# Optimization experiments

Measured on AMD Instinct MI355X. Metric: run time of the kernel, lower is better.

The kernel has to match this reference:

```python
import jax, jax.numpy as jnp
import numpy as np

N_CLASS, EMB, HID = 32000, 256, 512
B, T = 256, 256


def setup_inputs() -> dict:
    key = jax.random.key(0)
    ks = iter(jax.random.split(key, 64))

    def g(shape, scale=0.02):
        return jax.random.normal(next(ks), shape, jnp.float32) * scale

    inp = {
        "X": jax.random.randint(next(ks), (B, T), 0, N_CLASS),
        "H": g((B, HID)),
        "C": g((B, HID)),
        "E": g((N_CLASS, EMB)),
    }
    # two stacked LSTM cells, gates i/f/o/c; weights stored [in, out] so y = x @ W
    for name in ["i", "f", "o", "c"]:
        inp["W_x" + name] = g((EMB, HID))
        inp["W_h" + name] = g((HID, HID))
        inp["b_" + name] = jnp.ones((HID,), jnp.float32)
        inp["W_x" + name + "1"] = g((EMB, HID))
        inp["W_h" + name + "1"] = g((HID, HID))
        inp["b_" + name + "1"] = jnp.ones((HID,), jnp.float32)
    inp["W_xh"] = g((HID, HID))
    inp["W_hh"] = g((HID, HID))
    inp["b_h"] = jnp.ones((HID,), jnp.float32)
    inp["W_hq"] = g((HID, N_CLASS))
    inp["b_q"] = jnp.ones((N_CLASS,), jnp.float32)
    return inp


def reference(X, H, C, E,
              W_xi, W_hi, b_i, W_xf, W_hf, b_f, W_xo, W_ho, b_o, W_xc, W_hc, b_c,
              W_xi1, W_hi1, b_i1, W_xf1, W_hf1, b_f1, W_xo1, W_ho1, b_o1, W_xc1, W_hc1, b_c1,
              W_xh, W_hh, b_h, W_hq, b_q):
    xs = jnp.swapaxes(E[X], 0, 1)  # [T, B, EMB] time-major, like X.transpose(0,1)

    def step(carry, x_t):
        H, C, H1, C1 = carry
        # first LSTM cell
        I = jax.nn.sigmoid(x_t @ W_xi + H @ W_hi + b_i)
        F = jax.nn.sigmoid(x_t @ W_xf + H @ W_hf + b_f)
        O = jax.nn.sigmoid(x_t @ W_xo + H @ W_ho + b_o)
        Ct = jnp.tanh(x_t @ W_xc + H @ W_hc + b_c)
        C = F * C + I * Ct
        H = O * jnp.tanh(C)
        # inter-layer gated mix (note: H1 is overwritten before the 2nd cell, as in the original)
        H1 = jax.nn.sigmoid(H @ W_xh + H1 @ W_hh + b_h)
        # second LSTM cell
        I1 = jax.nn.sigmoid(x_t @ W_xi1 + H1 @ W_hi1 + b_i1)
        F1 = jax.nn.sigmoid(x_t @ W_xf1 + H1 @ W_hf1 + b_f1)
        O1 = jax.nn.sigmoid(x_t @ W_xo1 + H1 @ W_ho1 + b_o1)
        Ct1 = jnp.tanh(x_t @ W_xc1 + H1 @ W_hc1 + b_c1)
        C1 = F1 * C1 + I1 * Ct1
        H1 = O1 * jnp.tanh(C1)
        return (H, C, H1, C1), None

    # H1 and C1 are initialized from H and C (H1 = H; C1 = C in the original)
    (H, C, H1, C1), _ = jax.lax.scan(step, (H, C, H, C), xs)
    return H1 @ W_hq + b_q  # [B, N_CLASS]
```

## Files before the change

### kernel.cpp

```cpp
#include <hip/hip_runtime.h>
#include <cstdint>
#include <cstddef>

typedef unsigned short u16;
typedef unsigned long long u64;
typedef __attribute__((ext_vector_type(8))) short s16x8;
typedef __attribute__((ext_vector_type(4))) float f32x4;
typedef __attribute__((ext_vector_type(4))) unsigned short u16x4;

#define AGENT __HIP_MEMORY_SCOPE_AGENT

namespace {
constexpr int NWG  = 256;
constexpr int NTHR = 256;
constexpr int Bb   = 256;
constexpr int Tt   = 256;
constexpr int EMB_ = 256;
constexpr int HID_ = 512;
constexpr int NCLS = 32000;

constexpr int OFF_W1  = 0;
constexpr int OFF_W3  = 49152;
constexpr int OFF_W2  = 98304;
constexpr int OFF_DS  = 131072;
constexpr int OFF_DS1 = 139520;
constexpr int OFF_DSM = 147968;
constexpr int OFF_C   = 150144;
constexpr int OFF_C1  = 152192;
constexpr int OFF_B1  = 154240;
constexpr int OFF_B3  = 154368;
constexpr int OFF_B2  = 154496;
constexpr int SMEM_BYTES = 154560;

constexpr size_t WS_FL   = 0;
constexpr size_t WS_DONE = 32768;
constexpr size_t WS_HB0  = 33792;
constexpr size_t WS_HB1  = WS_HB0 + (size_t)Bb * HID_ * 2;
constexpr size_t WS_H1   = WS_HB1 + (size_t)Bb * HID_ * 2;
constexpr size_t WS_HM   = WS_H1 + (size_t)Bb * HID_ * 2;
constexpr size_t WS_XE   = WS_HM + (size_t)Bb * HID_ * 2;
}

struct Params {
  const int* X; const float* Hin; const float* Cin; const float* E;
  const float* Wx[4];  const float* Wh[4];  const float* bg[4];
  const float* Wx1[4]; const float* Wh1[4]; const float* bg1[4];
  const float* Wxh; const float* Whh; const float* bh;
  const float* Whq; const float* bq;
  float* out; char* ws;
};

__device__ __forceinline__ u16 f2bf(float f) {
  union { float f; unsigned u; } v; v.f = f;
  unsigned r = v.u + 0x7FFFu + ((v.u >> 16) & 1u);
  return (u16)(r >> 16);
}
__device__ __forceinline__ float sigm(float x) { return 1.f / (1.f + __expf(-x)); }
__device__ __forceinline__ float tanh_(float x) {
  x = fminf(fmaxf(x, -10.f), 10.f);
  float e = __expf(-2.f * x);
  return (1.f - e) / (1.f + e);
}
__device__ __forceinline__ f32x4 mfma16(s16x8 a, s16x8 b, f32x4 c) {
  return __builtin_amdgcn_mfma_f32_16x16x32_bf16(a, b, c, 0, 0, 0);
}

__device__ __forceinline__ void st8_llc(u16* p2, u64 v) {
  __hip_atomic_store((u64*)p2, v, __ATOMIC_RELAXED, AGENT);
}

#define LD16A(d, b, off)                                                      \
  asm volatile("global_load_dwordx4 %0, %1, off offset:" #off " sc0 sc1"      \
               : "=&v"(d) : "v"(b) : "memory")

__device__ __forceinline__ void ld_h16(s16x8* d, const u16* b) {
  LD16A(d[0],  b, 0);   LD16A(d[1],  b, 64);  LD16A(d[2],  b, 128);
  LD16A(d[3],  b, 192); LD16A(d[4],  b, 256); LD16A(d[5],  b, 320);
  LD16A(d[6],  b, 384); LD16A(d[7],  b, 448); LD16A(d[8],  b, 512);
  LD16A(d[9],  b, 576); LD16A(d[10], b, 640); LD16A(d[11], b, 704);
  LD16A(d[12], b, 768); LD16A(d[13], b, 832); LD16A(d[14], b, 896);
  LD16A(d[15], b, 960);
}
__device__ __forceinline__ void waitld() {
  asm volatile("s_waitcnt vmcnt(0)" ::: "memory");
  __builtin_amdgcn_sched_barrier(0);
}

__device__ __forceinline__ void arrive_cnt(int* fl, int c) {
  __syncthreads();
  if (threadIdx.x == 0)
    (void)__hip_atomic_fetch_add(&fl[(c & 7) * 32 + 16], 1, __ATOMIC_RELAXED, AGENT);
}
__device__ __forceinline__ void wait_cnt(int* fl, int ph) {
  const int tgt = ph * 8;
  if (threadIdx.x < 8) {
    for (;;) {
      int v = __hip_atomic_load(&fl[threadIdx.x * 32 + 16], __ATOMIC_RELAXED, AGENT);
      if (!__any(v < tgt)) break;
      __builtin_amdgcn_s_sleep(1);
    }
  }
  __syncthreads();
  __builtin_amdgcn_fence(__ATOMIC_ACQUIRE, "workgroup");
}

__device__ __forceinline__ void groupbar_heavy(int* fl, int slot, int ph) {
  __syncthreads();
  if (threadIdx.x == 0)
    __hip_atomic_store(&fl[slot * 32], ph, __ATOMIC_RELEASE, AGENT);
  if (threadIdx.x < 64) {
    for (;;) {
      int v = __hip_atomic_load(&fl[threadIdx.x * 32], __ATOMIC_RELAXED, AGENT);
      if (!__any(v < ph)) break;
      __builtin_amdgcn_s_sleep(1);
    }
  }
  __syncthreads();
  __builtin_amdgcn_fence(__ATOMIC_ACQUIRE, "agent");
}

__device__ __forceinline__ void donebar(int* dn, int bi) {
  __syncthreads();
  if (threadIdx.x == 0)
    __hip_atomic_store(&dn[bi], 1, __ATOMIC_RELEASE, AGENT);
  for (;;) {
    int v = __hip_atomic_load(&dn[threadIdx.x], __ATOMIC_RELAXED, AGENT);
    if (!__any(v < 1)) break;
    __builtin_amdgcn_s_sleep(1);
  }
  __syncthreads();
  __builtin_amdgcn_fence(__ATOMIC_ACQUIRE, "agent");
}

__device__ __forceinline__ void cell_phase(char* smem, int offW, int offB, int offC,
                                           const u16* Xt, const u16* Hrec, u16* Hdst,
                                           int g, int c, int w, int lane, int tid) {
  const int r = lane & 15, q = lane >> 4;
  const int row0 = w * 16;
  const u16* xrow = Xt + (size_t)(g * 64 + row0 + r) * EMB_;
  const u16* hrow = Hrec + (size_t)(g * 64 + row0 + r) * HID_;
  const u16* wb = (const u16*)(smem + offW) + lane * 8;
  f32x4 acc0 = {0.f, 0.f, 0.f, 0.f}, acc1 = {0.f, 0.f, 0.f, 0.f};
#pragma unroll
  for (int kb = 0; kb < 8; kb++) {
    s16x8 a  = *(const s16x8*)(xrow + kb * 32 + q * 8);
    s16x8 b0 = *(const s16x8*)(wb + (size_t)(kb * 2 + 0) * 512);
    s16x8 b1 = *(const s16x8*)(wb + (size_t)(kb * 2 + 1) * 512);
    acc0 = mfma16(a, b0, acc0);
    acc1 = mfma16(a, b1, acc1);
  }
  s16x8 ha[16];
  ld_h16(ha, hrow + q * 8);
  waitld();
#pragma unroll
  for (int kb = 0; kb < 16; kb++) {
    s16x8 b0 = *(const s16x8*)(wb + (size_t)((kb + 8) * 2 + 0) * 512);
    s16x8 b1 = *(const s16x8*)(wb + (size_t)((kb + 8) * 2 + 1) * 512);
    acc0 = mfma16(ha[kb], b0, acc0);
    acc1 = mfma16(ha[kb], b1, acc1);
  }
  float* Ds = (float*)(smem + OFF_DS);
#pragma unroll
  for (int i = 0; i < 4; i++) {
    Ds[(row0 + q * 4 + i) * 33 + r]      = acc0[i];
    Ds[(row0 + q * 4 + i) * 33 + 16 + r] = acc1[i];
  }
  __syncthreads();
  const float* bs = (const float*)(smem + offB);
  float* Cs = (float*)(smem + offC);
  if (tid < 128) {
    int row = tid >> 1, j0 = (tid & 1) * 4;
    union { u16 h[4]; u64 qv; } pk;
#pragma unroll
    for (int i = 0; i < 4; i++) {
      int j = j0 + i;
      float vi = Ds[row * 33 + 0 + j]  + bs[0 + j];
      float vf = Ds[row * 33 + 8 + j]  + bs[8 + j];
      float vo = Ds[row * 33 + 16 + j] + bs[16 + j];
      float vc = Ds[row * 33 + 24 + j] + bs[24 + j];
      float I = sigm(vi), F = sigm(vf), O = sigm(vo), Ct = tanh_(vc);
      float Cn = F * Cs[row * 8 + j] + I * Ct;
      Cs[row * 8 + j] = Cn;
      pk.h[i] = f2bf(O * tanh_(Cn));
    }
    st8_llc(Hdst + (size_t)(g * 64 + row) * HID_ + c * 8 + j0, pk.qv);
  }
}

__device__ __forceinline__ void cell1_w23(char* smem, const u16* Xt, const u16* Hrec,
                                          u16* Hdst, int g, int c, int lane, int tid) {
  const int wv = (tid >> 6) - 2;
  const int r = lane & 15, q = lane >> 4;
  const u16* wb1 = (const u16*)(smem + OFF_W1) + lane * 8;
  float* D1 = (float*)(smem + OFF_DS1);
#pragma unroll
  for (int blk = 0; blk < 2; blk++) {
    const int rb = wv * 32 + blk * 16;
    const u16* xrow = Xt + (size_t)(g * 64 + rb + r) * EMB_;
    const u16* hrow = Hrec + (size_t)(g * 64 + rb + r) * HID_;
    s16x8 xa[8];
#pragma unroll
    for (int kb = 0; kb < 8; kb++) xa[kb] = *(const s16x8*)(xrow + kb * 32 + q * 8);
    s16x8 hh[16];
    ld_h16(hh, hrow + q * 8);
    f32x4 a0 = {0.f, 0.f, 0.f, 0.f}, a1 = {0.f, 0.f, 0.f, 0.f};
#pragma unroll
    for (int kb = 0; kb < 8; kb++) {
      a0 = mfma16(xa[kb], *(const s16x8*)(wb1 + (size_t)(kb * 2 + 0) * 512), a0);
      a1 = mfma16(xa[kb], *(const s16x8*)(wb1 + (size_t)(kb * 2 + 1) * 512), a1);
    }
    waitld();
#pragma unroll
    for (int kb = 0; kb < 16; kb++) {
      a0 = mfma16(hh[kb], *(const s16x8*)(wb1 + (size_t)((kb + 8) * 2 + 0) * 512), a0);
      a1 = mfma16(hh[kb], *(const s16x8*)(wb1 + (size_t)((kb + 8) * 2 + 1) * 512), a1);
    }
#pragma unroll
    for (int i = 0; i < 4; i++) {
      D1[(rb + q * 4 + i) * 33 + r]      = a0[i];
      D1[(rb + q * 4 + i) * 33 + 16 + r] = a1[i];
    }
  }
  const float* bs = (const float*)(smem + OFF_B1);
  float* Cs = (float*)(smem + OFF_C);
  int t2 = tid - 128;
  int row = t2 >> 1, j0 = (t2 & 1) * 4;
  union { u16 h[4]; u64 qv; } pk;
#pragma unroll
  for (int i = 0; i < 4; i++) {
    int j = j0 + i;
    float vi = D1[row * 33 + 0 + j]  + bs[0 + j];
    float vf = D1[row * 33 + 8 + j]  + bs[8 + j];
    float vo = D1[row * 33 + 16 + j] + bs[16 + j];
    float vc = D1[row * 33 + 24 + j] + bs[24 + j];
    float I = sigm(vi), F = sigm(vf), O = sigm(vo), Ct = tanh_(vc);
    float Cn = F * Cs[row * 8 + j] + I * Ct;
    Cs[row * 8 + j] = Cn;
    pk.h[i] = f2bf(O * tanh_(Cn));
  }
  st8_llc(Hdst + (size_t)(g * 64 + row) * HID_ + c * 8 + j0, pk.qv);
}

__device__ __forceinline__ f32x4 mix_part1(char* smem, const u16* Hnew, int g, int c,
                                           int w, int lane) {
  const int r = lane & 15, q = lane >> 4;
  int rbase = g * 64 + (c & 1) * 32 + w * 16 + r;
  const u16* h0 = Hnew + (size_t)rbase * HID_;
  const u16* wb = (const u16*)(smem + OFF_W2) + lane * 8;
  s16x8 ha[16];
  ld_h16(ha, h0 + q * 8);
  waitld();
  f32x4 acc = {0.f, 0.f, 0.f, 0.f};
#pragma unroll
  for (int kb = 0; kb < 16; kb++)
    acc = mfma16(ha[kb], *(const s16x8*)(wb + (size_t)kb * 512), acc);
  return acc;
}

__device__ __forceinline__ void mix_part2(char* smem, f32x4 acc, const u16* H1old,
                                          u16* H1m, int g, int c, int w, int lane) {
  const int r = lane & 15, q = lane >> 4;
  int rbase = g * 64 + (c & 1) * 32 + w * 16 + r;
  const u16* h1 = H1old + (size_t)rbase * HID_;
  const u16* wb = (const u16*)(smem + OFF_W2) + lane * 8;
  s16x8 hb[16];
  ld_h16(hb, h1 + q * 8);
  waitld();
#pragma unroll
  for (int kb = 0; kb < 16; kb++)
    acc = mfma16(hb[kb], *(const s16x8*)(wb + (size_t)(16 + kb) * 512), acc);
  float* Dm = (float*)(smem + OFF_DSM) + (size_t)w * 16 * 17;
#pragma unroll
  for (int i = 0; i < 4; i++) Dm[(q * 4 + i) * 17 + r] = acc[i];
  const float* b2 = (const float*)(smem + OFF_B2);
  int row2 = lane >> 2, j0 = (lane & 3) * 4;
  union { u16 h[4]; u64 qv; } pk;
#pragma unroll
  for (int i = 0; i < 4; i++)
    pk.h[i] = f2bf(sigm(Dm[row2 * 17 + j0 + i] + b2[j0 + i]));
  st8_llc(H1m + (size_t)(g * 64 + (c & 1) * 32 + w * 16 + row2) * HID_ + (c >> 1) * 16 + j0,
          pk.qv);
}

__global__ __launch_bounds__(NTHR, 1) void lstm_pers(Params p) {
  extern __shared__ char smem[];
  const int tid = threadIdx.x;
  const int bi = blockIdx.x;
  const int w = tid >> 6, lane = tid & 63;
  const int g = bi >> 6, c = bi & 63;
  const int r = lane & 15, q = lane >> 4;

  int* fl = (int*)(p.ws + WS_FL) + g * 64 * 32;
  int* dn = (int*)(p.ws + WS_DONE);
  u16* Hb0 = (u16*)(p.ws + WS_HB0);
  u16* Hb1 = (u16*)(p.ws + WS_HB1);
  u16* H1b = (u16*)(p.ws + WS_H1);
  u16* H1m = (u16*)(p.ws + WS_HM);
  u16* Xe  = (u16*)(p.ws + WS_XE);

  if (tid == 0 && c < 8)
    __hip_atomic_store(&fl[c * 32 + 16], 0, __ATOMIC_RELAXED, AGENT);

  {
    u16* w1 = (u16*)(smem + OFF_W1);
    u16* w3 = (u16*)(smem + OFF_W3);
    int gate = tid >> 6, kk8 = (tid >> 3) & 7, j = tid & 7;
    int cc = gate * 8 + j;
    int n = cc >> 4, rr = cc & 15;
    int hid = c * 8 + j;
    for (int kk = kk8; kk < 768; kk += 8) {
      int kb = kk >> 5, q2 = (kk >> 3) & 3, e = kk & 7;
      size_t dst = ((size_t)(kb * 2 + n) * 64 + q2 * 16 + rr) * 8 + e;
      float s1 = (kk < 256) ? p.Wx[gate][(size_t)kk * HID_ + hid]
                            : p.Wh[gate][(size_t)(kk - 256) * HID_ + hid];
      float s3 = (kk < 256) ? p.Wx1[gate][(size_t)kk * HID_ + hid]
                            : p.Wh1[gate][(size_t)(kk - 256) * HID_ + hid];
      w1[dst] = f2bf(s1);
      w3[dst] = f2bf(s3);
    }
    {
      u16* w2 = (u16*)(smem + OFF_W2);
      int kk16 = tid >> 4, j2 = tid & 15;
      int hid2 = (c >> 1) * 16 + j2;
      for (int kk = kk16; kk < 1024; kk += 16) {
        int kb = kk >> 5, q2 = (kk >> 3) & 3, e = kk & 7;
        size_t dst = ((size_t)kb * 64 + q2 * 16 + j2) * 8 + e;
        float s = (kk < 512) ? p.Wxh[(size_t)kk * HID_ + hid2]
                             : p.Whh[(size_t)(kk - 512) * HID_ + hid2];
        w2[dst] = f2bf(s);
      }
      if (tid < 16) ((float*)(smem + OFF_B2))[tid] = p.bh[(c >> 1) * 16 + tid];
    }
    if (tid < 32) {
      int gt = tid >> 3, jj = tid & 7;
      ((float*)(smem + OFF_B1))[tid] = p.bg[gt][c * 8 + jj];
      ((float*)(smem + OFF_B3))[tid] = p.bg1[gt][c * 8 + jj];
    }
    float* Cs = (float*)(smem + OFF_C);
    float* C1s = (float*)(smem + OFF_C1);
    for (int it = 0; it < 2; it++) {
      int idx = tid + it * 256;
      int row = idx >> 3, j8 = idx & 7;
      float v = p.Cin[(size_t)(g * 64 + row) * HID_ + c * 8 + j8];
      Cs[row * 8 + j8] = v;
      C1s[row * 8 + j8] = v;
    }
  }
  for (int it = 0; it < 2; it++) {
    int idx = bi * 512 + tid + it * 256;
    u16 hv = f2bf(p.Hin[idx]);
    Hb1[idx] = hv;
    H1b[idx] = hv;
  }
  for (int tt = 0; tt < 4; tt++) {
    int t0 = c * 4 + tt;
    for (int pp = 0; pp < 16; pp++) {
      int b = g * 64 + w * 16 + pp;
      int tok = p.X[(size_t)b * Tt + t0];
      const float4* er = (const float4*)(p.E + (size_t)tok * EMB_);
      float4 v = er[lane];
      u16x4 u; u.x = f2bf(v.x); u.y = f2bf(v.y); u.z = f2bf(v.z); u.w = f2bf(v.w);
      *(u16x4*)(Xe + ((size_t)t0 * Bb + b) * EMB_ + lane * 4) = u;
    }
  }
  groupbar_heavy(fl, c, 1);

  int cph = 0;

  cell_phase(smem, OFF_W1, OFF_B1, OFF_C, Xe, Hb1, Hb0, g, c, w, lane, tid);
  arrive_cnt(fl, c); ++cph;

  wait_cnt(fl, cph);
  if (w < 2) {
    f32x4 macc = mix_part1(smem, Hb0, g, c, w, lane);
    mix_part2(smem, macc, H1b, H1m, g, c, w, lane);
  } else {
    cell1_w23(smem, Xe + (size_t)1 * Bb * EMB_, Hb0, Hb1, g, c, lane, tid);
  }
  arrive_cnt(fl, c); ++cph;

  for (int t = 0; t < Tt - 1; t++) {
    const u16* Xt = Xe + (size_t)t * Bb * EMB_;
    {
      const u16* wb3 = (const u16*)(smem + OFF_W3) + lane * 8;
      const u16* xrow = Xt + (size_t)(g * 64 + w * 16 + r) * EMB_;
      f32x4 acc0 = {0.f, 0.f, 0.f, 0.f}, acc1 = {0.f, 0.f, 0.f, 0.f};
      s16x8 xa[8];
#pragma unroll
      for (int kb = 0; kb < 8; kb++) xa[kb] = *(const s16x8*)(xrow + kb * 32 + q * 8);
#pragma unroll
      for (int kb = 0; kb < 8; kb++) {
        acc0 = mfma16(xa[kb], *(const s16x8*)(wb3 + (size_t)(kb * 2 + 0) * 512), acc0);
        acc1 = mfma16(xa[kb], *(const s16x8*)(wb3 + (size_t)(kb * 2 + 1) * 512), acc1);
      }
      wait_cnt(fl, cph);
      const u16* hrow = H1m + (size_t)(g * 64 + w * 16 + r) * HID_;
      s16x8 ha[16];
      ld_h16(ha, hrow + q * 8);
      waitld();
#pragma unroll
      for (int kb = 0; kb < 16; kb++) {
        acc0 = mfma16(ha[kb], *(const s16x8*)(wb3 + (size_t)((kb + 8) * 2 + 0) * 512), acc0);
        acc1 = mfma16(ha[kb], *(const s16x8*)(wb3 + (size_t)((kb + 8) * 2 + 1) * 512), acc1);
      }
      float* Ds = (float*)(smem + OFF_DS);
#pragma unroll
      for (int i = 0; i < 4; i++) {
        Ds[(w * 16 + q * 4 + i) * 33 + r]      = acc0[i];
        Ds[(w * 16 + q * 4 + i) * 33 + 16 + r] = acc1[i];
      }
      __syncthreads();
      if (tid < 128) {
        const float* bs = (const float*)(smem + OFF_B3);
        float* Cs = (float*)(smem + OFF_C1);
        int row = tid >> 1, j0 = (tid & 1) * 4;
        union { u16 h[4]; u64 qv; } pk;
#pragma unroll
        for (int i = 0; i < 4; i++) {
          int j = j0 + i;
          float vi = Ds[row * 33 + 0 + j]  + bs[0 + j];
          float vf = Ds[row * 33 + 8 + j]  + bs[8 + j];
          float vo = Ds[row * 33 + 16 + j] + bs[16 + j];
          float vc = Ds[row * 33 + 24 + j] + bs[24 + j];
          float I = sigm(vi), F = sigm(vf), O = sigm(vo), Ct = tanh_(vc);
          float Cn = F * Cs[row * 8 + j] + I * Ct;
          Cs[row * 8 + j] = Cn;
          pk.h[i] = f2bf(O * tanh_(Cn));
        }
        st8_llc(H1b + (size_t)(g * 64 + row) * HID_ + c * 8 + j0, pk.qv);
      }
      arrive_cnt(fl, c); ++cph;
    }
    {
      const u16* Hnew = (t & 1) ? Hb0 : Hb1;
      u16* Hdst1      = (t & 1) ? Hb1 : Hb0;
      f32x4 macc = {0.f, 0.f, 0.f, 0.f};
      if (w < 2) {
        macc = mix_part1(smem, Hnew, g, c, w, lane);
      } else if (t + 2 < Tt) {
        cell1_w23(smem, Xe + (size_t)(t + 2) * Bb * EMB_, Hnew, Hdst1, g, c, lane, tid);
      }
      wait_cnt(fl, cph);
      if (w < 2) mix_part2(smem, macc, H1b, H1m, g, c, w, lane);
      arrive_cnt(fl, c); ++cph;
    }
  }

  {
    const u16* Xt = Xe + (size_t)(Tt - 1) * Bb * EMB_;
    const u16* wb3 = (const u16*)(smem + OFF_W3) + lane * 8;
    const u16* xrow = Xt + (size_t)(g * 64 + w * 16 + r) * EMB_;
    f32x4 acc0 = {0.f, 0.f, 0.f, 0.f}, acc1 = {0.f, 0.f, 0.f, 0.f};
    s16x8 xa[8];
#pragma unroll
    for (int kb = 0; kb < 8; kb++) xa[kb] = *(const s16x8*)(xrow + kb * 32 + q * 8);
#pragma unroll
    for (int kb = 0; kb < 8; kb++) {
      acc0 = mfma16(xa[kb], *(const s16x8*)(wb3 + (size_t)(kb * 2 + 0) * 512), acc0);
      acc1 = mfma16(xa[kb], *(const s16x8*)(wb3 + (size_t)(kb * 2 + 1) * 512), acc1);
    }
    wait_cnt(fl, cph);
    const u16* hrow = H1m + (size_t)(g * 64 + w * 16 + r) * HID_;
    s16x8 ha[16];
    ld_h16(ha, hrow + q * 8);
    waitld();
#pragma unroll
    for (int kb = 0; kb < 16; kb++) {
      acc0 = mfma16(ha[kb], *(const s16x8*)(wb3 + (size_t)((kb + 8) * 2 + 0) * 512), acc0);
      acc1 = mfma16(ha[kb], *(const s16x8*)(wb3 + (size_t)((kb + 8) * 2 + 1) * 512), acc1);
    }
    float* Ds = (float*)(smem + OFF_DS);
#pragma unroll
    for (int i = 0; i < 4; i++) {
      Ds[(w * 16 + q * 4 + i) * 33 + r]      = acc0[i];
      Ds[(w * 16 + q * 4 + i) * 33 + 16 + r] = acc1[i];
    }
    __syncthreads();
    if (tid < 128) {
      const float* bs = (const float*)(smem + OFF_B3);
      float* Cs = (float*)(smem + OFF_C1);
      int row = tid >> 1, j0 = (tid & 1) * 4;
      union { u16 h[4]; u64 qv; } pk;
#pragma unroll
      for (int i = 0; i < 4; i++) {
        int j = j0 + i;
        float vi = Ds[row * 33 + 0 + j]  + bs[0 + j];
        float vf = Ds[row * 33 + 8 + j]  + bs[8 + j];
        float vo = Ds[row * 33 + 16 + j] + bs[16 + j];
        float vc = Ds[row * 33 + 24 + j] + bs[24 + j];
        float I = sigm(vi), F = sigm(vf), O = sigm(vo), Ct = tanh_(vc);
        float Cn = F * Cs[row * 8 + j] + I * Ct;
        Cs[row * 8 + j] = Cn;
        pk.h[i] = f2bf(O * tanh_(Cn));
      }
      st8_llc(H1b + (size_t)(g * 64 + row) * HID_ + c * 8 + j0, pk.qv);
    }
  }

  donebar(dn, bi);
  if (bi < 250) {
    const int n0 = bi * 128;
    u16* Wf = (u16*)smem;
    for (int idx = tid; idx < 512 * 128; idx += NTHR) {
      int k = idx >> 7, nn2 = idx & 127;
      int nt = nn2 >> 4, rr = nn2 & 15;
      int kb = k >> 5, q2 = (k >> 3) & 3, e = k & 7;
      Wf[((size_t)(kb * 8 + nt) * 64 + q2 * 16 + rr) * 8 + e] =
          f2bf(p.Whq[(size_t)k * NCLS + n0 + nn2]);
    }
    float* bqs = (float*)(smem + OFF_C);
    if (tid < 128) bqs[tid] = p.bq[n0 + tid];
    __syncthreads();
    const int r2 = lane & 15, q2 = lane >> 4;
    for (int mt = 0; mt < 4; mt++) {
      int rowb = mt * 64 + w * 16;
      const u16* arow = H1b + (size_t)(rowb + r2) * HID_;
      f32x4 acc[8];
#pragma unroll
      for (int nt = 0; nt < 8; nt++) acc[nt] = (f32x4){0.f, 0.f, 0.f, 0.f};
      for (int kb = 0; kb < 16; kb++) {
        s16x8 a = *(const s16x8*)(arow + kb * 32 + q2 * 8);
#pragma unroll
        for (int nt = 0; nt < 8; nt++) {
          s16x8 b = *(const s16x8*)((const u16*)Wf + ((size_t)(kb * 8 + nt) * 64 + lane) * 8);
          acc[nt] = mfma16(a, b, acc[nt]);
        }
      }
#pragma unroll
      for (int nt = 0; nt < 8; nt++)
#pragma unroll
        for (int i = 0; i < 4; i++)
          p.out[(size_t)(rowb + q2 * 4 + i) * NCLS + n0 + nt * 16 + r2] =
              acc[nt][i] + bqs[nt * 16 + r2];
    }
  }
}

extern "C" void kernel_launch(void* const* d_in, const int* in_sizes, int n_in,
                              void* d_out, int out_size, void* d_ws, size_t ws_size,
                              hipStream_t stream) {
  (void)in_sizes; (void)n_in; (void)out_size; (void)ws_size;
  Params p;
  p.X   = (const int*)d_in[0];
  p.Hin = (const float*)d_in[1];
  p.Cin = (const float*)d_in[2];
  p.E   = (const float*)d_in[3];
  for (int gidx = 0; gidx < 4; gidx++) {
    int base = 4 + gidx * 6;
    p.Wx[gidx]  = (const float*)d_in[base + 0];
    p.Wh[gidx]  = (const float*)d_in[base + 1];
    p.bg[gidx]  = (const float*)d_in[base + 2];
    p.Wx1[gidx] = (const float*)d_in[base + 3];
    p.Wh1[gidx] = (const float*)d_in[base + 4];
    p.bg1[gidx] = (const float*)d_in[base + 5];
  }
  p.Wxh = (const float*)d_in[28];
  p.Whh = (const float*)d_in[29];
  p.bh  = (const float*)d_in[30];
  p.Whq = (const float*)d_in[31];
  p.bq  = (const float*)d_in[32];
  p.out = (float*)d_out;
  p.ws  = (char*)d_ws;

  hipFuncSetAttribute(reinterpret_cast<const void*>(lstm_pers),
                      hipFuncAttributeMaxDynamicSharedMemorySize, SMEM_BYTES);
  lstm_pers<<<dim3(NWG), dim3(NTHR), SMEM_BYTES, stream>>>(p);
}
```

Before: 3.554 ms.

## Split group barrier into per-wave dependency counters for cell, mix and output phases

```diff
diff --git a/kernel.cpp b/kernel.cpp
--- a/kernel.cpp
+++ b/kernel.cpp
@@ -32,6 +32,7 @@
 constexpr int OFF_B2  = 154496;
 constexpr int SMEM_BYTES = 154560;
 
+constexpr int LA = 0, LM = 8, LC = 16;
 constexpr size_t WS_FL   = 0;
 constexpr size_t WS_DONE = 32768;
 constexpr size_t WS_HB0  = 33792;
@@ -86,22 +87,27 @@
   __builtin_amdgcn_sched_barrier(0);
 }
 
-__device__ __forceinline__ void arrive_cnt(int* fl, int c) {
+__device__ __forceinline__ void wait_wave(int* fl, int lineBase, int tgt) {
+  const int lane = threadIdx.x & 63;
+  for (;;) {
+    int v = __hip_atomic_load(&fl[(lineBase + (lane & 7)) * 32 + 16],
+                              __ATOMIC_RELAXED, AGENT);
+    if (!__any(v < tgt)) break;
+    __builtin_amdgcn_s_sleep(1);
+  }
+  __builtin_amdgcn_fence(__ATOMIC_ACQUIRE, "workgroup");
+}
+__device__ __forceinline__ void arrive_wave(int* fl, int lineBase, int c) {
+  asm volatile("s_waitcnt vmcnt(0)" ::: "memory");
+  if ((threadIdx.x & 63) == 0)
+    (void)__hip_atomic_fetch_add(&fl[(lineBase + (c & 7)) * 32 + 16], 1,
+                                 __ATOMIC_RELAXED, AGENT);
+}
+__device__ __forceinline__ void arrive_all(int* fl, int lineBase, int c) {
   __syncthreads();
   if (threadIdx.x == 0)
-    (void)__hip_atomic_fetch_add(&fl[(c & 7) * 32 + 16], 1, __ATOMIC_RELAXED, AGENT);
-}
-__device__ __forceinline__ void wait_cnt(int* fl, int ph) {
-  const int tgt = ph * 8;
-  if (threadIdx.x < 8) {
-    for (;;) {
-      int v = __hip_atomic_load(&fl[threadIdx.x * 32 + 16], __ATOMIC_RELAXED, AGENT);
-      if (!__any(v < tgt)) break;
-      __builtin_amdgcn_s_sleep(1);
-    }
-  }
-  __syncthreads();
-  __builtin_amdgcn_fence(__ATOMIC_ACQUIRE, "workgroup");
+    (void)__hip_atomic_fetch_add(&fl[(lineBase + (c & 7)) * 32 + 16], 1,
+                                 __ATOMIC_RELAXED, AGENT);
 }
 
 __device__ __forceinline__ void groupbar_heavy(int* fl, int slot, int ph) {
@@ -298,7 +304,7 @@
   u16* H1m = (u16*)(p.ws + WS_HM);
   u16* Xe  = (u16*)(p.ws + WS_XE);
 
-  if (tid == 0 && c < 8)
+  if (tid == 0 && c < 24)
     __hip_atomic_store(&fl[c * 32 + 16], 0, __ATOMIC_RELAXED, AGENT);
 
   {
@@ -365,19 +371,19 @@
   }
   groupbar_heavy(fl, c, 1);
 
-  int cph = 0;
 
   cell_phase(smem, OFF_W1, OFF_B1, OFF_C, Xe, Hb1, Hb0, g, c, w, lane, tid);
-  arrive_cnt(fl, c); ++cph;
-
-  wait_cnt(fl, cph);
+  if (w < 2) arrive_wave(fl, LC, c);
+
+  wait_wave(fl, LC, 1 * 16);
   if (w < 2) {
     f32x4 macc = mix_part1(smem, Hb0, g, c, w, lane);
     mix_part2(smem, macc, H1b, H1m, g, c, w, lane);
+    arrive_wave(fl, LM, c);
   } else {
     cell1_w23(smem, Xe + (size_t)1 * Bb * EMB_, Hb0, Hb1, g, c, lane, tid);
-  }
-  arrive_cnt(fl, c); ++cph;
+    arrive_wave(fl, LC, c);
+  }
 
   for (int t = 0; t < Tt - 1; t++) {
     const u16* Xt = Xe + (size_t)t * Bb * EMB_;
@@ -393,7 +399,8 @@
         acc0 = mfma16(xa[kb], *(const s16x8*)(wb3 + (size_t)(kb * 2 + 0) * 512), acc0);
         acc1 = mfma16(xa[kb], *(const s16x8*)(wb3 + (size_t)(kb * 2 + 1) * 512), acc1);
       }
-      wait_cnt(fl, cph);
+      wait_wave(fl, LM, (t + 1) * 16);
+      __syncthreads();
       const u16* hrow = H1m + (size_t)(g * 64 + w * 16 + r) * HID_;
       s16x8 ha[16];
       ld_h16(ha, hrow + q * 8);
@@ -429,20 +436,21 @@
         }
         st8_llc(H1b + (size_t)(g * 64 + row) * HID_ + c * 8 + j0, pk.qv);
       }
-      arrive_cnt(fl, c); ++cph;
+      arrive_all(fl, LA, c);
     }
     {
       const u16* Hnew = (t & 1) ? Hb0 : Hb1;
       u16* Hdst1      = (t & 1) ? Hb1 : Hb0;
-      f32x4 macc = {0.f, 0.f, 0.f, 0.f};
+      wait_wave(fl, LC, (t + 2) * 16);
       if (w < 2) {
-        macc = mix_part1(smem, Hnew, g, c, w, lane);
+        f32x4 macc = mix_part1(smem, Hnew, g, c, w, lane);
+        wait_wave(fl, LA, (t + 1) * 8);
+        mix_part2(smem, macc, H1b, H1m, g, c, w, lane);
+        arrive_wave(fl, LM, c);
       } else if (t + 2 < Tt) {
         cell1_w23(smem, Xe + (size_t)(t + 2) * Bb * EMB_, Hnew, Hdst1, g, c, lane, tid);
-      }
-      wait_cnt(fl, cph);
-      if (w < 2) mix_part2(smem, macc, H1b, H1m, g, c, w, lane);
-      arrive_cnt(fl, c); ++cph;
+        arrive_wave(fl, LC, c);
+      }
     }
   }
 
@@ -459,7 +467,8 @@
       acc0 = mfma16(xa[kb], *(const s16x8*)(wb3 + (size_t)(kb * 2 + 0) * 512), acc0);
       acc1 = mfma16(xa[kb], *(const s16x8*)(wb3 + (size_t)(kb * 2 + 1) * 512), acc1);
     }
-    wait_cnt(fl, cph);
+    wait_wave(fl, LM, Tt * 16);
+    __syncthreads();
     const u16* hrow = H1m + (size_t)(g * 64 + w * 16 + r) * HID_;
     s16x8 ha[16];
     ld_h16(ha, hrow + q * 8);
```

Measured after the change: 3.964 ms. +11.5%, slower.
